# Performance work log

Hardware: AMD Instinct MI355X
Metric: run time of the kernel (lower is better)

Reference implementation:

```python
import jax, jax.numpy as jnp
import numpy as np

N = 50000      # nodes
E = 600000     # directed edges
F_IN = 11      # node features (QM9-like)
G = 512        # graphs in batch
TGT = 12


def _lin(key, fi, fo):
    kw, kb = jax.random.split(key)
    s = 1.0 / np.sqrt(fi)
    W = jax.random.uniform(kw, (fi, fo), jnp.float32, -s, s)
    b = jax.random.uniform(kb, (fo,), jnp.float32, -s, s)
    return W, b


def setup_inputs() -> dict:
    key = jax.random.key(0)
    ks = jax.random.split(key, 9)
    x = jax.random.normal(ks[0], (N, F_IN), jnp.float32)
    edge_index = jax.random.randint(ks[1], (2, E), 0, N, dtype=jnp.int32)
    batch = jnp.sort(jax.random.randint(ks[2], (N,), 0, G, dtype=jnp.int32))
    W1, b1 = _lin(ks[3], F_IN, 32)
    W2, b2 = _lin(ks[4], 32, 64)
    W3, b3 = _lin(ks[5], 64, 128)
    fw1, fb1 = _lin(ks[6], 128, 64)
    fw2, fb2 = _lin(ks[7], 64, TGT)
    return {"x": x, "edge_index": edge_index, "batch": batch,
            "W1": W1, "b1": b1, "W2": W2, "b2": b2, "W3": W3, "b3": b3,
            "fw1": fw1, "fb1": fb1, "fw2": fw2, "fb2": fb2}


def reference(x, edge_index, batch, W1, b1, W2, b2, W3, b3, fw1, fb1, fw2, fb2):
    src, dst = edge_index[0], edge_index[1]
    n = x.shape[0]
    # GCN symmetric normalization with self-loops: deg counts incoming edges + 1
    deg = 1.0 + jax.ops.segment_sum(jnp.ones(src.shape[0], x.dtype), dst, num_segments=n)
    dis = jax.lax.rsqrt(deg)                      # deg^{-1/2}, [N]
    edge_norm = dis[src] * dis[dst]               # [E]

    def gcn_conv(h, W, b):
        hw = h @ W                                # [N, Fo]
        agg = jax.ops.segment_sum(hw[src] * edge_norm[:, None], dst, num_segments=n)
        # self-loop contribution: deg^{-1} * hw
        return agg + hw * (dis * dis)[:, None] + b

    h = jax.nn.relu(gcn_conv(x, W1, b1))
    h = jax.nn.relu(gcn_conv(h, W2, b2))
    h = gcn_conv(h, W3, b3)                       # no relu before pooling (matches source)

    # global_mean_pool over batch ids
    sums = jax.ops.segment_sum(h, batch, num_segments=G)
    counts = jax.ops.segment_sum(jnp.ones(n, h.dtype), batch, num_segments=G)
    pooled = sums / jnp.maximum(counts, 1.0)[:, None]

    h = jax.nn.relu(pooled @ fw1 + fb1)
    return h @ fw2 + fb2
```

## Files before the change

### kernel.cpp

```cpp
#include <hip/hip_runtime.h>
#include <hip/hip_bf16.h>
#include <hip/hip_fp16.h>


#define GG 512
#define TGT 12

union F4H8 { float4 f4; __half2 h2[4]; };

__device__ __forceinline__ void acc_add_h8(float* acc, float4 raw) {
    F4H8 u; u.f4 = raw;
#pragma unroll
    for (int k = 0; k < 4; ++k) {
        float2 f = __half22float2(u.h2[k]);
        acc[2 * k] += f.x;
        acc[2 * k + 1] += f.y;
    }
}


__global__ void zero_kernel(int4* __restrict__ p, int n4) {
    int i = blockIdx.x * blockDim.x + threadIdx.x;
    if (i < n4) p[i] = make_int4(0, 0, 0, 0);
}


__global__ void deg_count_kernel(const int* __restrict__ dst, int* __restrict__ cnt, int E) {
    int i = blockIdx.x * blockDim.x + threadIdx.x;
    if (i < E) atomicAdd(&cnt[dst[i]], 1);
}


__global__ void dis_scale_kernel(const int* __restrict__ cnt, const float* __restrict__ x,
                                 float* __restrict__ dis, float* __restrict__ hs, int n) {
    long long idx = (long long)blockIdx.x * blockDim.x + threadIdx.x;
    int node = (int)(idx >> 4);
    int lane = (int)(idx & 15);
    if (node >= n) return;
    float d = rsqrtf(1.0f + (float)cnt[node]);
    if (lane == 0) dis[node] = d;
    hs[(size_t)node * 16 + lane] = (lane < 11) ? x[(size_t)node * 11 + lane] * d : 0.0f;
}


__global__ void scan1_kernel(const int* __restrict__ cnt, int* __restrict__ excl,
                             int* __restrict__ psum, int n) {
    __shared__ int sh[256];
    int i = blockIdx.x * 256 + threadIdx.x;
    int v = (i < n) ? cnt[i] : 0;
    sh[threadIdx.x] = v;
    __syncthreads();
    for (int off = 1; off < 256; off <<= 1) {
        int t = (threadIdx.x >= (unsigned)off) ? sh[threadIdx.x - off] : 0;
        __syncthreads();
        sh[threadIdx.x] += t;
        __syncthreads();
    }
    if (i < n) excl[i] = sh[threadIdx.x] - v;
    if (threadIdx.x == 255) psum[blockIdx.x] = sh[255];
}

__global__ void scan2_kernel(int* __restrict__ psum, int nb) {
    __shared__ int sh[256];
    int carry = 0;
    for (int base = 0; base < nb; base += 256) {
        int i = base + threadIdx.x;
        int v = (i < nb) ? psum[i] : 0;
        sh[threadIdx.x] = v;
        __syncthreads();
        for (int off = 1; off < 256; off <<= 1) {
            int t = (threadIdx.x >= (unsigned)off) ? sh[threadIdx.x - off] : 0;
            __syncthreads();
            sh[threadIdx.x] += t;
            __syncthreads();
        }
        if (i < nb) psum[i] = sh[threadIdx.x] - v + carry;
        carry += sh[255];
        __syncthreads();
    }
}


__global__ void place_kernel(const int* __restrict__ src, const int* __restrict__ dst,
                             const int* __restrict__ excl, const int* __restrict__ psum,
                             int* __restrict__ incnt, int* __restrict__ esrc, int E) {
    int i = blockIdx.x * blockDim.x + threadIdx.x;
    if (i < E) {
        int d = dst[i];
        int r = atomicSub(&incnt[d], 1) - 1;
        int pos = excl[d] + psum[d >> 8] + r;
        esrc[pos] = src[i];
    }
}

__device__ __forceinline__ int offs_of(const int* __restrict__ excl,
                                       const int* __restrict__ psum, int i) {
    return excl[i] + psum[i >> 8];
}


template <int F, int FI, int FO>
__global__ void aggemm_f32_kernel(const float4* __restrict__ hs, const float* __restrict__ dis,
                                  const int* __restrict__ excl, const int* __restrict__ psum,
                                  const int* __restrict__ esrc,
                                  const float* __restrict__ W, const float* __restrict__ b,
                                  __half* __restrict__ out, int n, int Etot) {
    constexpr int LP = F / 4;
    constexpr int NPB = 256 / LP;
    __shared__ float srow[NPB][F];
    __shared__ float sdn[NPB];
    __shared__ float sW[FI * FO];
    for (int i = threadIdx.x; i < FI * FO; i += 256) sW[i] = W[i];

    int nd = threadIdx.x / LP;
    int lane = threadIdx.x % LP;
    int node = blockIdx.x * NPB + nd;
    if (node < n) {
        float4 acc = hs[(size_t)node * LP + lane];
        int s0 = offs_of(excl, psum, node);
        int send = (node + 1 < n) ? offs_of(excl, psum, node + 1) : Etot;
        int c = send - s0;
        int e = 0;
        for (; e + 2 <= c; e += 2) {
            int sa = esrc[s0 + e], sb = esrc[s0 + e + 1];
            float4 va = hs[(size_t)sa * LP + lane];
            float4 vb = hs[(size_t)sb * LP + lane];
            acc.x += va.x + vb.x; acc.y += va.y + vb.y;
            acc.z += va.z + vb.z; acc.w += va.w + vb.w;
        }
        if (e < c) {
            int sa = esrc[s0 + e];
            float4 va = hs[(size_t)sa * LP + lane];
            acc.x += va.x; acc.y += va.y; acc.z += va.z; acc.w += va.w;
        }
        float dn = dis[node];
        srow[nd][lane * 4 + 0] = acc.x * dn;
        srow[nd][lane * 4 + 1] = acc.y * dn;
        srow[nd][lane * 4 + 2] = acc.z * dn;
        srow[nd][lane * 4 + 3] = acc.w * dn;
        if (lane == 0) sdn[nd] = dn;
    }
    __syncthreads();

    int base = blockIdx.x * NPB;
    for (int o = threadIdx.x; o < NPB * FO; o += 256) {
        int fo = o % FO;
        int nd2 = o / FO;
        int node2 = base + nd2;
        if (node2 < n) {
            float acc = b[fo];
#pragma unroll
            for (int fi = 0; fi < FI; ++fi) acc += srow[nd2][fi] * sW[fi * FO + fo];
            out[(size_t)node2 * FO + fo] = __float2half(fmaxf(acc, 0.0f) * sdn[nd2]);
        }
    }
}


template <int F, int FI, int FO>
__global__ void aggemm_h_kernel(const float4* __restrict__ hs, const float* __restrict__ dis,
                                const int* __restrict__ excl, const int* __restrict__ psum,
                                const int* __restrict__ esrc,
                                const float* __restrict__ W, const float* __restrict__ b,
                                __half* __restrict__ out, int n, int Etot) {
    constexpr int LP = F / 8;
    constexpr int NPB = 256 / LP;
    __shared__ float srow[NPB][F];
    __shared__ float sdn[NPB];
    __shared__ float sW[FI * FO];
    for (int i = threadIdx.x; i < FI * FO; i += 256) sW[i] = W[i];

    int nd = threadIdx.x / LP;
    int lane = threadIdx.x % LP;
    int node = blockIdx.x * NPB + nd;
    if (node < n) {
        float acc[8] = {0, 0, 0, 0, 0, 0, 0, 0};
        acc_add_h8(acc, hs[(size_t)node * LP + lane]);
        int s0 = offs_of(excl, psum, node);
        int send = (node + 1 < n) ? offs_of(excl, psum, node + 1) : Etot;
        int c = send - s0;
        int e = 0;
        for (; e + 2 <= c; e += 2) {
            int sa = esrc[s0 + e], sb = esrc[s0 + e + 1];
            float4 va = hs[(size_t)sa * LP + lane];
            float4 vb = hs[(size_t)sb * LP + lane];
            acc_add_h8(acc, va);
            acc_add_h8(acc, vb);
        }
        if (e < c) acc_add_h8(acc, hs[(size_t)esrc[s0 + e] * LP + lane]);
        float dn = dis[node];
#pragma unroll
        for (int j = 0; j < 8; ++j) srow[nd][lane * 8 + j] = acc[j] * dn;
        if (lane == 0) sdn[nd] = dn;
    }
    __syncthreads();

    int base = blockIdx.x * NPB;
    for (int o = threadIdx.x; o < NPB * FO; o += 256) {
        int fo = o % FO;
        int nd2 = o / FO;
        int node2 = base + nd2;
        if (node2 < n) {
            float acc = b[fo];
#pragma unroll
            for (int fi = 0; fi < FI; ++fi) acc += srow[nd2][fi] * sW[fi * FO + fo];
            out[(size_t)node2 * FO + fo] = __float2half(fmaxf(acc, 0.0f) * sdn[nd2]);
        }
    }
}


__global__ void agg64h_kernel(const float4* __restrict__ hs, const float* __restrict__ dis,
                              const int* __restrict__ excl, const int* __restrict__ psum,
                              const int* __restrict__ esrc, float4* __restrict__ out,
                              int n, int Etot) {
    constexpr int LP = 8;
    constexpr int NPB = 32;
    int node = blockIdx.x * NPB + (int)(threadIdx.x / LP);
    int lane = threadIdx.x % LP;
    if (node >= n) return;
    float acc[8] = {0, 0, 0, 0, 0, 0, 0, 0};
    acc_add_h8(acc, hs[(size_t)node * LP + lane]);
    int s0 = offs_of(excl, psum, node);
    int send = (node + 1 < n) ? offs_of(excl, psum, node + 1) : Etot;
    int c = send - s0;
    int e = 0;
    for (; e + 2 <= c; e += 2) {
        int sa = esrc[s0 + e], sb = esrc[s0 + e + 1];
        float4 va = hs[(size_t)sa * LP + lane];
        float4 vb = hs[(size_t)sb * LP + lane];
        acc_add_h8(acc, va);
        acc_add_h8(acc, vb);
    }
    if (e < c) acc_add_h8(acc, hs[(size_t)esrc[s0 + e] * LP + lane]);
    float dn = dis[node];
    F4H8 w;
#pragma unroll
    for (int k = 0; k < 4; ++k)
        w.h2[k] = __float22half2_rn(make_float2(acc[2 * k] * dn, acc[2 * k + 1] * dn));
    out[(size_t)node * LP + lane] = w.f4;
}


__global__ void poolhead_kernel(const __half* __restrict__ h, const int* __restrict__ batch,
                                const float* __restrict__ W3, const float* __restrict__ b3,
                                const float* __restrict__ fw1, const float* __restrict__ fb1,
                                const float* __restrict__ fw2, const float* __restrict__ fb2,
                                float* __restrict__ out, int n) {
    int g = blockIdx.x;
    auto lb = [&](int key) {
        int lo = 0, hi = n;
        while (lo < hi) {
            int mid = (lo + hi) >> 1;
            if (batch[mid] < key) lo = mid + 1; else hi = mid;
        }
        return lo;
    };
    int lo = lb(g), hi = lb(g + 1);
    float c = (float)(hi - lo);
    float inv = (c > 0.0f) ? 1.0f / c : 0.0f;

    __shared__ float red[4][64];
    __shared__ float sp[64];
    __shared__ float p128[128];
    __shared__ float h64[64];

    int fo = threadIdx.x & 63;
    int sub = threadIdx.x >> 6;
    float acc = 0.0f;
    for (int i = lo + sub; i < hi; i += 4) acc += __half2float(h[(size_t)i * 64 + fo]);
    red[sub][fo] = acc;
    __syncthreads();
    if (sub == 0) sp[fo] = (red[0][fo] + red[1][fo] + red[2][fo] + red[3][fo]) * inv;
    __syncthreads();

    int j = threadIdx.x;
    if (j < 128) {
        float a = (c > 0.0f) ? b3[j] : 0.0f;
#pragma unroll
        for (int k = 0; k < 64; ++k) a += sp[k] * W3[k * 128 + j];
        p128[j] = a;
    }
    __syncthreads();
    if (j < 64) {
        float a = fb1[j];
#pragma unroll
        for (int k = 0; k < 128; ++k) a += p128[k] * fw1[k * 64 + j];
        h64[j] = fmaxf(a, 0.0f);
    }
    __syncthreads();
    if (j < TGT) {
        float a = fb2[j];
#pragma unroll
        for (int k = 0; k < 64; ++k) a += h64[k] * fw2[k * TGT + j];
        out[(size_t)g * TGT + j] = a;
    }
}

extern "C" void kernel_launch(void* const* d_in, const int* in_sizes, int n_in,
                              void* d_out, int out_size, void* d_ws, size_t ws_size,
                              hipStream_t stream) {
    const float* x = (const float*)d_in[0];
    const int* edge_index = (const int*)d_in[1];
    const int* batch = (const int*)d_in[2];
    const float* W1 = (const float*)d_in[3];
    const float* b1 = (const float*)d_in[4];
    const float* W2 = (const float*)d_in[5];
    const float* b2 = (const float*)d_in[6];
    const float* W3 = (const float*)d_in[7];
    const float* b3 = (const float*)d_in[8];
    const float* fw1 = (const float*)d_in[9];
    const float* fb1 = (const float*)d_in[10];
    const float* fw2 = (const float*)d_in[11];
    const float* fb2 = (const float*)d_in[12];
    float* out = (float*)d_out;

    const int N = in_sizes[2];
    const int E = in_sizes[1] / 2;
    const int* src = edge_index;
    const int* dst = edge_index + E;

    int* incnt = (int*)d_ws;
    int* excl = incnt + N;
    int* psum = excl + N;
    int* esrc = psum + 256;
    float* dis = (float*)(esrc + E);
    float* hx = dis + N;
    __half* h1 = (__half*)(hx + (size_t)N * 16);
    __half* h2 = h1 + (size_t)N * 32;
    __half* h3 = h2 + (size_t)N * 64;

    const int T = 256;
    auto cdiv = [](long long a, long long b) { return (int)((a + b - 1) / b); };
    const int nb1 = cdiv(N, 256);

    zero_kernel<<<cdiv(cdiv(N, 4), T), T, 0, stream>>>((int4*)incnt, cdiv(N, 4));
    deg_count_kernel<<<cdiv(E, T), T, 0, stream>>>(dst, incnt, E);
    dis_scale_kernel<<<cdiv((long long)N * 16, T), T, 0, stream>>>(incnt, x, dis, hx, N);
    scan1_kernel<<<nb1, 256, 0, stream>>>(incnt, excl, psum, N);
    scan2_kernel<<<1, 256, 0, stream>>>(psum, nb1);
    place_kernel<<<cdiv(E, T), T, 0, stream>>>(src, dst, excl, psum, incnt, esrc, E);

    aggemm_f32_kernel<16, 11, 32><<<cdiv(N, 64), T, 0, stream>>>(
        (const float4*)hx, dis, excl, psum, esrc, W1, b1, h1, N, E);

    aggemm_h_kernel<32, 32, 64><<<cdiv(N, 64), T, 0, stream>>>(
        (const float4*)h1, dis, excl, psum, esrc, W2, b2, h2, N, E);

    agg64h_kernel<<<cdiv(N, 32), T, 0, stream>>>(
        (const float4*)h2, dis, excl, psum, esrc, (float4*)h3, N, E);
    poolhead_kernel<<<GG, 256, 0, stream>>>(h3, batch, W3, b3, fw1, fb1, fw2, fb2, out, N);
}
```

Baseline: 148.2 us.

## Fuse layer-3 aggregation with mean pooling and merge prep kernels

New measurement: 138.3 us. -6.7%, faster.

```diff
diff --git a/kernel.cpp b/kernel.cpp
--- a/kernel.cpp
+++ b/kernel.cpp
@@ -1,5 +1,4 @@
 #include <hip/hip_runtime.h>
-#include <hip/hip_bf16.h>
 #include <hip/hip_fp16.h>
 
 
@@ -8,56 +7,53 @@
 
 union F4H8 { float4 f4; __half2 h2[4]; };
 
-__device__ __forceinline__ void acc_add_h8(float* acc, float4 raw) {
+__device__ __forceinline__ void acc_add_h8(float* a, float4 raw) {
     F4H8 u; u.f4 = raw;
 #pragma unroll
     for (int k = 0; k < 4; ++k) {
         float2 f = __half22float2(u.h2[k]);
-        acc[2 * k] += f.x;
-        acc[2 * k + 1] += f.y;
-    }
-}
-
+        a[2 * k] += f.x;
+        a[2 * k + 1] += f.y;
+    }
+}
 
 __global__ void zero_kernel(int4* __restrict__ p, int n4) {
     int i = blockIdx.x * blockDim.x + threadIdx.x;
     if (i < n4) p[i] = make_int4(0, 0, 0, 0);
 }
 
-
 __global__ void deg_count_kernel(const int* __restrict__ dst, int* __restrict__ cnt, int E) {
     int i = blockIdx.x * blockDim.x + threadIdx.x;
     if (i < E) atomicAdd(&cnt[dst[i]], 1);
 }
 
 
-__global__ void dis_scale_kernel(const int* __restrict__ cnt, const float* __restrict__ x,
-                                 float* __restrict__ dis, float* __restrict__ hs, int n) {
-    long long idx = (long long)blockIdx.x * blockDim.x + threadIdx.x;
-    int node = (int)(idx >> 4);
-    int lane = (int)(idx & 15);
-    if (node >= n) return;
-    float d = rsqrtf(1.0f + (float)cnt[node]);
-    if (lane == 0) dis[node] = d;
-    hs[(size_t)node * 16 + lane] = (lane < 11) ? x[(size_t)node * 11 + lane] * d : 0.0f;
-}
-
-
-__global__ void scan1_kernel(const int* __restrict__ cnt, int* __restrict__ excl,
-                             int* __restrict__ psum, int n) {
-    __shared__ int sh[256];
-    int i = blockIdx.x * 256 + threadIdx.x;
-    int v = (i < n) ? cnt[i] : 0;
-    sh[threadIdx.x] = v;
-    __syncthreads();
-    for (int off = 1; off < 256; off <<= 1) {
-        int t = (threadIdx.x >= (unsigned)off) ? sh[threadIdx.x - off] : 0;
+__global__ void prep_kernel(const int* __restrict__ cnt, const float* __restrict__ x,
+                            float* __restrict__ dis, float* __restrict__ hs,
+                            int* __restrict__ excl, int* __restrict__ psum, int n, int nb1) {
+    int gid = blockIdx.x * 256 + threadIdx.x;
+    int gstride = gridDim.x * 256;
+    for (int idx = gid; idx < n * 16; idx += gstride) {
+        int node = idx >> 4, lane = idx & 15;
+        float d = rsqrtf(1.0f + (float)cnt[node]);
+        if (lane == 0) dis[node] = d;
+        hs[idx] = (lane < 11) ? x[node * 11 + lane] * d : 0.0f;
+    }
+    if (blockIdx.x < nb1) {
+        __shared__ int sh[256];
+        int i = blockIdx.x * 256 + threadIdx.x;
+        int v = (i < n) ? cnt[i] : 0;
+        sh[threadIdx.x] = v;
         __syncthreads();
-        sh[threadIdx.x] += t;
-        __syncthreads();
-    }
-    if (i < n) excl[i] = sh[threadIdx.x] - v;
-    if (threadIdx.x == 255) psum[blockIdx.x] = sh[255];
+        for (int off = 1; off < 256; off <<= 1) {
+            int t = (threadIdx.x >= (unsigned)off) ? sh[threadIdx.x - off] : 0;
+            __syncthreads();
+            sh[threadIdx.x] += t;
+            __syncthreads();
+        }
+        if (i < n) excl[i] = sh[threadIdx.x] - v;
+        if (threadIdx.x == 255) psum[blockIdx.x] = sh[255];
+    }
 }
 
 __global__ void scan2_kernel(int* __restrict__ psum, int nb) {
@@ -80,7 +76,6 @@
     }
 }
 
-
 __global__ void place_kernel(const int* __restrict__ src, const int* __restrict__ dst,
                              const int* __restrict__ excl, const int* __restrict__ psum,
                              int* __restrict__ incnt, int* __restrict__ esrc, int E) {
@@ -88,8 +83,7 @@
     if (i < E) {
         int d = dst[i];
         int r = atomicSub(&incnt[d], 1) - 1;
-        int pos = excl[d] + psum[d >> 8] + r;
-        esrc[pos] = src[i];
+        esrc[excl[d] + psum[d >> 8] + r] = src[i];
     }
 }
 
@@ -99,154 +93,167 @@
 }
 
 
-template <int F, int FI, int FO>
-__global__ void aggemm_f32_kernel(const float4* __restrict__ hs, const float* __restrict__ dis,
-                                  const int* __restrict__ excl, const int* __restrict__ psum,
-                                  const int* __restrict__ esrc,
-                                  const float* __restrict__ W, const float* __restrict__ b,
-                                  __half* __restrict__ out, int n, int Etot) {
-    constexpr int LP = F / 4;
-    constexpr int NPB = 256 / LP;
-    __shared__ float srow[NPB][F];
-    __shared__ float sdn[NPB];
-    __shared__ float sW[FI * FO];
-    for (int i = threadIdx.x; i < FI * FO; i += 256) sW[i] = W[i];
-
-    int nd = threadIdx.x / LP;
-    int lane = threadIdx.x % LP;
-    int node = blockIdx.x * NPB + nd;
+__global__ void aggemm1_kernel(const float4* __restrict__ hp, const float* __restrict__ dis,
+                               const int* __restrict__ excl, const int* __restrict__ psum,
+                               const int* __restrict__ esrc,
+                               const float* __restrict__ W, const float* __restrict__ b,
+                               __half* __restrict__ out, int n, int Etot) {
+    __shared__ float srow[64 * 16];
+    __shared__ float sdn[64];
+    __shared__ float sW[11 * 32];
+    for (int i = threadIdx.x; i < 11 * 32; i += 256) sW[i] = W[i];
+
+    int nd = threadIdx.x >> 2, lane = threadIdx.x & 3;
+    int node = blockIdx.x * 64 + nd;
     if (node < n) {
-        float4 acc = hs[(size_t)node * LP + lane];
         int s0 = offs_of(excl, psum, node);
         int send = (node + 1 < n) ? offs_of(excl, psum, node + 1) : Etot;
         int c = send - s0;
+        float4 A = hp[(size_t)node * 4 + lane];
+        float4 B = make_float4(0, 0, 0, 0);
         int e = 0;
-        for (; e + 2 <= c; e += 2) {
+        for (; e + 4 <= c; e += 4) {
             int sa = esrc[s0 + e], sb = esrc[s0 + e + 1];
-            float4 va = hs[(size_t)sa * LP + lane];
-            float4 vb = hs[(size_t)sb * LP + lane];
-            acc.x += va.x + vb.x; acc.y += va.y + vb.y;
-            acc.z += va.z + vb.z; acc.w += va.w + vb.w;
-        }
-        if (e < c) {
-            int sa = esrc[s0 + e];
-            float4 va = hs[(size_t)sa * LP + lane];
-            acc.x += va.x; acc.y += va.y; acc.z += va.z; acc.w += va.w;
+            int sc = esrc[s0 + e + 2], sd = esrc[s0 + e + 3];
+            float4 va = hp[(size_t)sa * 4 + lane], vb = hp[(size_t)sb * 4 + lane];
+            float4 vc = hp[(size_t)sc * 4 + lane], vd = hp[(size_t)sd * 4 + lane];
+            A.x += va.x + vb.x; A.y += va.y + vb.y; A.z += va.z + vb.z; A.w += va.w + vb.w;
+            B.x += vc.x + vd.x; B.y += vc.y + vd.y; B.z += vc.z + vd.z; B.w += vc.w + vd.w;
+        }
+        for (; e < c; ++e) {
+            float4 va = hp[(size_t)esrc[s0 + e] * 4 + lane];
+            A.x += va.x; A.y += va.y; A.z += va.z; A.w += va.w;
         }
         float dn = dis[node];
-        srow[nd][lane * 4 + 0] = acc.x * dn;
-        srow[nd][lane * 4 + 1] = acc.y * dn;
-        srow[nd][lane * 4 + 2] = acc.z * dn;
-        srow[nd][lane * 4 + 3] = acc.w * dn;
+        srow[nd * 16 + lane * 4 + 0] = (A.x + B.x) * dn;
+        srow[nd * 16 + lane * 4 + 1] = (A.y + B.y) * dn;
+        srow[nd * 16 + lane * 4 + 2] = (A.z + B.z) * dn;
+        srow[nd * 16 + lane * 4 + 3] = (A.w + B.w) * dn;
         if (lane == 0) sdn[nd] = dn;
     }
     __syncthreads();
 
-    int base = blockIdx.x * NPB;
-    for (int o = threadIdx.x; o < NPB * FO; o += 256) {
-        int fo = o % FO;
-        int nd2 = o / FO;
+    int base = blockIdx.x * 64;
+    for (int o = threadIdx.x; o < 64 * 32; o += 256) {
+        int fo = o & 31, nd2 = o >> 5;
         int node2 = base + nd2;
         if (node2 < n) {
-            float acc = b[fo];
-#pragma unroll
-            for (int fi = 0; fi < FI; ++fi) acc += srow[nd2][fi] * sW[fi * FO + fo];
-            out[(size_t)node2 * FO + fo] = __float2half(fmaxf(acc, 0.0f) * sdn[nd2]);
-        }
-    }
-}
-
-
-template <int F, int FI, int FO>
-__global__ void aggemm_h_kernel(const float4* __restrict__ hs, const float* __restrict__ dis,
-                                const int* __restrict__ excl, const int* __restrict__ psum,
-                                const int* __restrict__ esrc,
-                                const float* __restrict__ W, const float* __restrict__ b,
-                                __half* __restrict__ out, int n, int Etot) {
-    constexpr int LP = F / 8;
-    constexpr int NPB = 256 / LP;
-    __shared__ float srow[NPB][F];
-    __shared__ float sdn[NPB];
-    __shared__ float sW[FI * FO];
-    for (int i = threadIdx.x; i < FI * FO; i += 256) sW[i] = W[i];
-
-    int nd = threadIdx.x / LP;
-    int lane = threadIdx.x % LP;
-    int node = blockIdx.x * NPB + nd;
+            float a = b[fo];
+#pragma unroll
+            for (int fi = 0; fi < 11; ++fi) a += srow[nd2 * 16 + fi] * sW[fi * 32 + fo];
+            out[(size_t)node2 * 32 + fo] = __float2half(fmaxf(a, 0.0f) * sdn[nd2]);
+        }
+    }
+}
+
+
+__global__ void aggemm2_kernel(const float4* __restrict__ hp, const float* __restrict__ dis,
+                               const int* __restrict__ excl, const int* __restrict__ psum,
+                               const int* __restrict__ esrc,
+                               const float* __restrict__ W, const float* __restrict__ b,
+                               __half* __restrict__ out, int n, int Etot) {
+    __shared__ float srow[64 * 32];
+    __shared__ float sdn[64];
+    __shared__ float sW[32 * 64];
+    for (int i = threadIdx.x; i < 32 * 64; i += 256) sW[i] = W[i];
+
+    int nd = threadIdx.x >> 2, lane = threadIdx.x & 3;
+    int node = blockIdx.x * 64 + nd;
     if (node < n) {
-        float acc[8] = {0, 0, 0, 0, 0, 0, 0, 0};
-        acc_add_h8(acc, hs[(size_t)node * LP + lane]);
         int s0 = offs_of(excl, psum, node);
         int send = (node + 1 < n) ? offs_of(excl, psum, node + 1) : Etot;
         int c = send - s0;
+        float accA[8] = {0, 0, 0, 0, 0, 0, 0, 0};
+        float accB[8] = {0, 0, 0, 0, 0, 0, 0, 0};
+        acc_add_h8(accA, hp[(size_t)node * 4 + lane]);
         int e = 0;
-        for (; e + 2 <= c; e += 2) {
+        for (; e + 4 <= c; e += 4) {
             int sa = esrc[s0 + e], sb = esrc[s0 + e + 1];
-            float4 va = hs[(size_t)sa * LP + lane];
-            float4 vb = hs[(size_t)sb * LP + lane];
-            acc_add_h8(acc, va);
-            acc_add_h8(acc, vb);
-        }
-        if (e < c) acc_add_h8(acc, hs[(size_t)esrc[s0 + e] * LP + lane]);
+            int sc = esrc[s0 + e + 2], sd = esrc[s0 + e + 3];
+            float4 va = hp[(size_t)sa * 4 + lane], vb = hp[(size_t)sb * 4 + lane];
+            float4 vc = hp[(size_t)sc * 4 + lane], vd = hp[(size_t)sd * 4 + lane];
+            acc_add_h8(accA, va); acc_add_h8(accB, vb);
+            acc_add_h8(accA, vc); acc_add_h8(accB, vd);
+        }
+        for (; e < c; ++e) acc_add_h8(accA, hp[(size_t)esrc[s0 + e] * 4 + lane]);
         float dn = dis[node];
 #pragma unroll
-        for (int j = 0; j < 8; ++j) srow[nd][lane * 8 + j] = acc[j] * dn;
+        for (int j = 0; j < 8; ++j) srow[nd * 32 + lane * 8 + j] = (accA[j] + accB[j]) * dn;
         if (lane == 0) sdn[nd] = dn;
     }
     __syncthreads();
 
-    int base = blockIdx.x * NPB;
-    for (int o = threadIdx.x; o < NPB * FO; o += 256) {
-        int fo = o % FO;
-        int nd2 = o / FO;
+    int base = blockIdx.x * 64;
+    for (int o = threadIdx.x; o < 64 * 64; o += 256) {
+        int fo = o & 63, nd2 = o >> 6;
         int node2 = base + nd2;
         if (node2 < n) {
-            float acc = b[fo];
-#pragma unroll
-            for (int fi = 0; fi < FI; ++fi) acc += srow[nd2][fi] * sW[fi * FO + fo];
-            out[(size_t)node2 * FO + fo] = __float2half(fmaxf(acc, 0.0f) * sdn[nd2]);
-        }
-    }
-}
-
-
-__global__ void agg64h_kernel(const float4* __restrict__ hs, const float* __restrict__ dis,
-                              const int* __restrict__ excl, const int* __restrict__ psum,
-                              const int* __restrict__ esrc, float4* __restrict__ out,
-                              int n, int Etot) {
-    constexpr int LP = 8;
-    constexpr int NPB = 32;
-    int node = blockIdx.x * NPB + (int)(threadIdx.x / LP);
-    int lane = threadIdx.x % LP;
-    if (node >= n) return;
-    float acc[8] = {0, 0, 0, 0, 0, 0, 0, 0};
-    acc_add_h8(acc, hs[(size_t)node * LP + lane]);
-    int s0 = offs_of(excl, psum, node);
-    int send = (node + 1 < n) ? offs_of(excl, psum, node + 1) : Etot;
-    int c = send - s0;
-    int e = 0;
-    for (; e + 2 <= c; e += 2) {
-        int sa = esrc[s0 + e], sb = esrc[s0 + e + 1];
-        float4 va = hs[(size_t)sa * LP + lane];
-        float4 vb = hs[(size_t)sb * LP + lane];
-        acc_add_h8(acc, va);
-        acc_add_h8(acc, vb);
-    }
-    if (e < c) acc_add_h8(acc, hs[(size_t)esrc[s0 + e] * LP + lane]);
-    float dn = dis[node];
-    F4H8 w;
-#pragma unroll
-    for (int k = 0; k < 4; ++k)
-        w.h2[k] = __float22half2_rn(make_float2(acc[2 * k] * dn, acc[2 * k + 1] * dn));
-    out[(size_t)node * LP + lane] = w.f4;
-}
-
-
-__global__ void poolhead_kernel(const __half* __restrict__ h, const int* __restrict__ batch,
-                                const float* __restrict__ W3, const float* __restrict__ b3,
-                                const float* __restrict__ fw1, const float* __restrict__ fb1,
-                                const float* __restrict__ fw2, const float* __restrict__ fb2,
-                                float* __restrict__ out, int n) {
+            float a = b[fo];
+#pragma unroll
+            for (int fi = 0; fi < 32; ++fi) a += srow[nd2 * 32 + fi] * sW[fi * 64 + fo];
+            out[(size_t)node2 * 64 + fo] = __float2half(fmaxf(a, 0.0f) * sdn[nd2]);
+        }
+    }
+}
+
+
+__global__ void agg64pool_kernel(const float4* __restrict__ hp, const float* __restrict__ dis,
+                                 const int* __restrict__ excl, const int* __restrict__ psum,
+                                 const int* __restrict__ esrc, const int* __restrict__ batch,
+                                 float* __restrict__ pooled, int n, int Etot) {
+    __shared__ float srow[32 * 64];
+    int nd = threadIdx.x >> 3, lane = threadIdx.x & 7;
+    int base = blockIdx.x * 32;
+    int node = base + nd;
+    if (node < n) {
+        int s0 = offs_of(excl, psum, node);
+        int send = (node + 1 < n) ? offs_of(excl, psum, node + 1) : Etot;
+        int c = send - s0;
+        float accA[8] = {0, 0, 0, 0, 0, 0, 0, 0};
+        float accB[8] = {0, 0, 0, 0, 0, 0, 0, 0};
+        acc_add_h8(accA, hp[(size_t)node * 8 + lane]);
+        int e = 0;
+        for (; e + 4 <= c; e += 4) {
+            int sa = esrc[s0 + e], sb = esrc[s0 + e + 1];
+            int sc = esrc[s0 + e + 2], sd = esrc[s0 + e + 3];
+            float4 va = hp[(size_t)sa * 8 + lane], vb = hp[(size_t)sb * 8 + lane];
+            float4 vc = hp[(size_t)sc * 8 + lane], vd = hp[(size_t)sd * 8 + lane];
+            acc_add_h8(accA, va); acc_add_h8(accB, vb);
+            acc_add_h8(accA, vc); acc_add_h8(accB, vd);
+        }
+        for (; e < c; ++e) acc_add_h8(accA, hp[(size_t)esrc[s0 + e] * 8 + lane]);
+        float dn = dis[node];
+#pragma unroll
+        for (int j = 0; j < 8; ++j) srow[nd * 64 + lane * 8 + j] = (accA[j] + accB[j]) * dn;
+    } else {
+#pragma unroll
+        for (int j = 0; j < 8; ++j) srow[nd * 64 + lane * 8 + j] = 0.0f;
+    }
+    __syncthreads();
+
+    int fo = threadIdx.x & 63, q = threadIdx.x >> 6;
+    float acc = 0.0f;
+    int gcur = -1;
+    for (int k = 0; k < 8; ++k) {
+        int node2 = base + q * 8 + k;
+        if (node2 >= n) break;
+        int g = batch[node2];
+        if (g != gcur) {
+            if (gcur >= 0) atomicAdd(&pooled[(size_t)gcur * 64 + fo], acc);
+            acc = 0.0f;
+            gcur = g;
+        }
+        acc += srow[(q * 8 + k) * 64 + fo];
+    }
+    if (gcur >= 0) atomicAdd(&pooled[(size_t)gcur * 64 + fo], acc);
+}
+
+
+__global__ void head_kernel(const float* __restrict__ pooled, const int* __restrict__ batch,
+                            const float* __restrict__ W3, const float* __restrict__ b3,
+                            const float* __restrict__ fw1, const float* __restrict__ fb1,
+                            const float* __restrict__ fw2, const float* __restrict__ fb2,
+                            float* __restrict__ out, int n) {
     int g = blockIdx.x;
     auto lb = [&](int key) {
         int lo = 0, hi = n;
@@ -260,22 +267,13 @@
     float c = (float)(hi - lo);
     float inv = (c > 0.0f) ? 1.0f / c : 0.0f;
 
-    __shared__ float red[4][64];
     __shared__ float sp[64];
     __shared__ float p128[128];
     __shared__ float h64[64];
-
-    int fo = threadIdx.x & 63;
-    int sub = threadIdx.x >> 6;
-    float acc = 0.0f;
-    for (int i = lo + sub; i < hi; i += 4) acc += __half2float(h[(size_t)i * 64 + fo]);
-    red[sub][fo] = acc;
-    __syncthreads();
-    if (sub == 0) sp[fo] = (red[0][fo] + red[1][fo] + red[2][fo] + red[3][fo]) * inv;
-    __syncthreads();
-
     int j = threadIdx.x;
-    if (j < 128) {
+    if (j < 64) sp[j] = pooled[(size_t)g * 64 + j] * inv;
+    __syncthreads();
+    {
         float a = (c > 0.0f) ? b3[j] : 0.0f;
 #pragma unroll
         for (int k = 0; k < 64; ++k) a += sp[k] * W3[k * 128 + j];
@@ -321,33 +319,31 @@
     const int* dst = edge_index + E;
 
     int* incnt = (int*)d_ws;
-    int* excl = incnt + N;
+    float* pooled = (float*)(incnt + N);
+    int* excl = (int*)(pooled + GG * 64);
     int* psum = excl + N;
     int* esrc = psum + 256;
     float* dis = (float*)(esrc + E);
     float* hx = dis + N;
     __half* h1 = (__half*)(hx + (size_t)N * 16);
     __half* h2 = h1 + (size_t)N * 32;
-    __half* h3 = h2 + (size_t)N * 64;
 
     const int T = 256;
     auto cdiv = [](long long a, long long b) { return (int)((a + b - 1) / b); };
     const int nb1 = cdiv(N, 256);
 
-    zero_kernel<<<cdiv(cdiv(N, 4), T), T, 0, stream>>>((int4*)incnt, cdiv(N, 4));
+    const int zero_ints = N + GG * 64;
+    zero_kernel<<<cdiv(cdiv(zero_ints, 4), T), T, 0, stream>>>((int4*)d_ws, cdiv(zero_ints, 4));
     deg_count_kernel<<<cdiv(E, T), T, 0, stream>>>(dst, incnt, E);
-    dis_scale_kernel<<<cdiv((long long)N * 16, T), T, 0, stream>>>(incnt, x, dis, hx, N);
-    scan1_kernel<<<nb1, 256, 0, stream>>>(incnt, excl, psum, N);
+    prep_kernel<<<cdiv((long long)N * 16, T), T, 0, stream>>>(incnt, x, dis, hx, excl, psum, N, nb1);
     scan2_kernel<<<1, 256, 0, stream>>>(psum, nb1);
     place_kernel<<<cdiv(E, T), T, 0, stream>>>(src, dst, excl, psum, incnt, esrc, E);
 
-    aggemm_f32_kernel<16, 11, 32><<<cdiv(N, 64), T, 0, stream>>>(
+    aggemm1_kernel<<<cdiv(N, 64), T, 0, stream>>>(
         (const float4*)hx, dis, excl, psum, esrc, W1, b1, h1, N, E);
-
-    aggemm_h_kernel<32, 32, 64><<<cdiv(N, 64), T, 0, stream>>>(
+    aggemm2_kernel<<<cdiv(N, 64), T, 0, stream>>>(
         (const float4*)h1, dis, excl, psum, esrc, W2, b2, h2, N, E);
-
-    agg64h_kernel<<<cdiv(N, 32), T, 0, stream>>>(
-        (const float4*)h2, dis, excl, psum, esrc, (float4*)h3, N, E);
-    poolhead_kernel<<<GG, 256, 0, stream>>>(h3, batch, W3, b3, fw1, fb1, fw2, fb2, out, N);
-}
+    agg64pool_kernel<<<cdiv(N, 32), T, 0, stream>>>(
+        (const float4*)h2, dis, excl, psum, esrc, batch, pooled, N, E);
+    head_kernel<<<GG, 128, 0, stream>>>(pooled, batch, W3, b3, fw1, fb1, fw2, fb2, out, N);
+}
```
